# Kernel optimization log

Measured on AMD Instinct MI355X. Metric: run time of the kernel, lower is better.

## Reference

```python
import jax, jax.numpy as jnp
import numpy as np

N = 16384
C_IN = 128
C_OUT = 128
S_DIM = 4
P_DIM = 32
K = 16


def setup_inputs() -> dict:
    key = jax.random.key(0)
    ks = jax.random.split(key, 8)
    lim = lambda fan_in: 1.0 / np.sqrt(fan_in)
    u = lambda k_, shape, b: jax.random.uniform(k_, shape, jnp.float32, -b, b)
    return {
        "x": jax.random.normal(ks[0], (N, C_IN), jnp.float32),
        "Ws": u(ks[1], (S_DIM, C_IN), lim(C_IN)),
        "bs": u(ks[2], (S_DIM,), lim(C_IN)),
        "Wh": u(ks[3], (P_DIM, C_IN), lim(C_IN)),
        "bh": u(ks[4], (P_DIM,), lim(C_IN)),
        "W1": u(ks[5], (C_OUT, C_IN), lim(C_IN)),
        "W2": u(ks[6], (C_OUT, 2 * P_DIM), lim(2 * P_DIM)),
        "b2": u(ks[7], (C_OUT,), lim(2 * P_DIM)),
        "k": K,
    }


def reference(x, Ws, bs, Wh, bh, W1, W2, b2, k):
    # latent space positions and message vectors
    s = x @ Ws.T + bs            # [N, S]
    h = x @ Wh.T + bh            # [N, P]
    # squared-distance matrix via Gram trick (monotone in true distance,
    # so k-NN indices match torch.cdist + topk(largest=False))
    sq = jnp.sum(s * s, axis=-1)                         # [N]
    d2 = sq[:, None] + sq[None, :] - 2.0 * (s @ s.T)     # [N, N]
    _, idx = jax.lax.top_k(-d2, k)                       # [N, k] neighbour ids (incl. self)
    # exact squared latent distance to selected neighbours (as in torch code)
    s_j = s[idx]                                          # [N, k, S]
    w = jnp.exp(-10.0 * jnp.sum((s[:, None, :] - s_j) ** 2, axis=-1))  # [N, k]
    msg = h[idx] * w[..., None]                           # [N, k, P]
    agg = jnp.concatenate([msg.mean(axis=1), msg.max(axis=1)], axis=-1)  # [N, 2P]
    return x @ W1.T + agg @ W2.T + b2                     # [N, C_OUT]
```

## Files before the change

### kernel.cpp

```cpp
#include <hip/hip_runtime.h>
#include <hip/hip_bf16.h>


#define NPTS 16384
#define CIN  128
#define SD   4
#define PD   32
#define KNN  16
#define COUT 128
#define FLTMAX 3.4028234663852886e+38f
#define NBIN 33
#define QPB  8
#define QCAP 512
#define MCAP 192
#define EPAD 1e-3f

typedef float v2f __attribute__((ext_vector_type(2)));
typedef unsigned int uint;
typedef unsigned long long u64;
typedef unsigned short u16;
typedef __attribute__((ext_vector_type(8))) short bf16x8;
typedef __attribute__((ext_vector_type(16))) float f32x16;

#define WS_S4     0
#define WS_H      0x40000
#define WS_AGG_M  0x280000
#define WS_SA     0x280000
#define WS_SB     0x300000
#define WS_WT_M   0x680000
#define WS_MASK   0x700000
#define WS_NEED_M 0x2700000
#define WS_CJ_F   0x400000
#define WS_AGG_F  0xC00000
#define WS_WT_F   0x1000000
#define JS   16
#define TJF  (NPTS/JS)

__device__ __forceinline__ float d2f(const float4 a, const float4 b) {
  v2f d0 = {a.x - b.x, a.y - b.y};
  v2f d1 = {a.z - b.z, a.w - b.w};
  v2f pr = d0*d0 + d1*d1;
  return pr.x + pr.y;
}

__device__ __forceinline__ u16 f2bf(float x) {
  uint u = __float_as_uint(x);
  uint r = (u + 0x7FFFu + ((u >> 16) & 1u)) >> 16;
  return (u16)r;
}
__device__ __forceinline__ float bf2f(u16 h) {
  return __uint_as_float(((uint)h) << 16);
}

__global__ __launch_bounds__(256) void k1_proj(
    const float* __restrict__ x, const float* __restrict__ Ws, const float* __restrict__ bs,
    const float* __restrict__ Wh, const float* __restrict__ bh,
    float4* __restrict__ s4, float* __restrict__ h) {
  __shared__ float  lw[36*128];
  __shared__ float  lx[64*132];
  __shared__ double rs[3*64*5];
  __shared__ float  rh[3*64*33];
  const int t = threadIdx.x;
  const int row0 = blockIdx.x * 64;
  for (int i2 = t; i2 < 36*128; i2 += 256)
    lw[i2] = (i2 < 512) ? Ws[i2] : Wh[i2 - 512];
#pragma unroll
  for (int g = 0; g < 8; ++g) {
    int fi = g*256 + t;
    int r = fi >> 5, c4 = fi & 31;
    *(float4*)&lx[r*132 + c4*4] = *(const float4*)&x[(size_t)(row0 + r)*CIN + c4*4];
  }
  __syncthreads();
  const int kq = t >> 6;
  const int r  = t & 63;
  const int kb = kq * 32;
  double sacc[4] = {0.0, 0.0, 0.0, 0.0};
  float  hacc[32];
#pragma unroll
  for (int p = 0; p < 32; ++p) hacc[p] = 0.f;
#pragma unroll
  for (int k4 = 0; k4 < 8; ++k4) {
    float4 xv = *(const float4*)&lx[r*132 + kb + k4*4];
    int kg = kb + k4*4;
#pragma unroll
    for (int p = 0; p < 4; ++p) {
      float4 wv = *(const float4*)&lw[p*128 + kg];
      sacc[p] = fma((double)xv.x, (double)wv.x, sacc[p]);
      sacc[p] = fma((double)xv.y, (double)wv.y, sacc[p]);
      sacc[p] = fma((double)xv.z, (double)wv.z, sacc[p]);
      sacc[p] = fma((double)xv.w, (double)wv.w, sacc[p]);
    }
#pragma unroll
    for (int p = 0; p < 32; ++p) {
      float4 wv = *(const float4*)&lw[(4+p)*128 + kg];
      hacc[p] = fmaf(xv.x, wv.x, fmaf(xv.y, wv.y, fmaf(xv.z, wv.z, fmaf(xv.w, wv.w, hacc[p]))));
    }
  }
  if (kq > 0) {
    const int bq = kq - 1;
#pragma unroll
    for (int d = 0; d < 4; ++d) rs[(bq*64 + r)*5 + d] = sacc[d];
#pragma unroll
    for (int p = 0; p < 32; ++p) rh[(bq*64 + r)*33 + p] = hacc[p];
  }
  __syncthreads();
  if (kq == 0) {
    const int row = row0 + r;
    float so[4];
#pragma unroll
    for (int d = 0; d < 4; ++d) {
      double sd = sacc[d] + rs[(0*64 + r)*5 + d] + rs[(1*64 + r)*5 + d]
                + rs[(2*64 + r)*5 + d] + (double)bs[d];
      so[d] = (float)sd;
    }
    s4[row] = make_float4(so[0], so[1], so[2], so[3]);
#pragma unroll
    for (int p4 = 0; p4 < 8; ++p4) {
      float o[4];
#pragma unroll
      for (int c = 0; c < 4; ++c) {
        int p = p4*4 + c;
        o[c] = hacc[p] + rh[(0*64 + r)*33 + p] + rh[(1*64 + r)*33 + p]
             + rh[(2*64 + r)*33 + p] + bh[p];
      }
      *(float4*)&h[(size_t)row*PD + p4*4] = make_float4(o[0], o[1], o[2], o[3]);
    }
  }
}

__global__ __launch_bounds__(256) void k2t_thresh(
    const float4* __restrict__ s4, uint4* __restrict__ sA, uint4* __restrict__ sB) {
  __shared__ float4 tile[2064];
  __shared__ uint   lhist[256*NBIN];
  const int t = threadIdx.x;
#pragma unroll
  for (int g = 0; g < 8; ++g) {
    int j = g*256 + t;
    tile[j + (j >> 7)] = s4[j];
  }
#pragma unroll
  for (int b = 0; b < NBIN; ++b) lhist[t*NBIN + b] = 0u;
  const int ql = t >> 4, tq = t & 15;
  const int q  = blockIdx.x*16 + ql;
  const float4 sq = s4[q];
  __syncthreads();
  float tau = d2f(sq, tile[tq*129]);
#pragma unroll
  for (int m = 1; m < 16; m <<= 1) tau = fmaxf(tau, __shfl_xor(tau, m, 16));
  const int ktop = (int)(__float_as_uint(tau) >> 21);
  const int hb = t*NBIN;
#pragma unroll 4
  for (int u = 0; u < 128; ++u) {
    float4 p = tile[tq*129 + u];
    float e = d2f(sq, p);
    int key = (int)(__float_as_uint(e) >> 21);
    int rel = ktop - key;
    rel = rel < 0 ? 0 : (rel > 32 ? 32 : rel);
    atomicAdd(&lhist[hb + rel], 1u);
  }
  __syncthreads();
  uint c0 = 0, c1 = 0;
  const int qb = ql*16;
  for (int u = 0; u < 16; ++u) {
    c0 += lhist[(qb + u)*NBIN + tq*2];
    c1 += (tq*2 + 1 < NBIN) ? lhist[(qb + u)*NBIN + tq*2 + 1] : 0u;
  }
  int S = (int)(c0 + c1);
#pragma unroll
  for (int d = 1; d < 16; d <<= 1) {
    int v = __shfl_down(S, d, 16);
    S += (tq + d < 16) ? v : 0;
  }
  int g = -1;
  if (S >= KNN) g = 2*tq;
  if (S - (int)c0 >= KNN) g = 2*tq + 1;
#pragma unroll
  for (int m = 1; m < 16; m <<= 1) g = max(g, __shfl_xor(g, m, 16));
  if (tq == 0) {
    uint K = (uint)(ktop - g);
    const float tv = __uint_as_float((K << 21) | 0x1FFFFFu);
    float sv[4] = {sq.x, sq.y, sq.z, sq.w};
    const float n2 = sq.x*sq.x + sq.y*sq.y + sq.z*sq.z + sq.w*sq.w;
    u16 hbv[4], lbv[4];
#pragma unroll
    for (int d = 0; d < 4; ++d) {
      u16 hh = f2bf(sv[d]);
      hbv[d] = hh;
      lbv[d] = f2bf(sv[d] - bf2f(hh));
    }
    const float aq = -0.5f*(n2 - tv) + EPAD;
    const float bn = -0.5f*n2;
    u16 aqh = f2bf(aq); u16 aql = f2bf(aq - bf2f(aqh));
    u16 bnh = f2bf(bn); u16 bnl = f2bf(bn - bf2f(bnh));
    const uint oneone = 0x3F803F80u;
    uint a0 = (uint)hbv[0] | ((uint)hbv[1] << 16);
    uint a1 = (uint)hbv[2] | ((uint)hbv[3] << 16);
    uint l0 = (uint)lbv[0] | ((uint)lbv[1] << 16);
    uint l1 = (uint)lbv[2] | ((uint)lbv[3] << 16);
    uint aqw = (uint)aqh | ((uint)aql << 16);
    uint bnw = (uint)bnh | ((uint)bnl << 16);
    uint4 A0; A0.x = a0; A0.y = a1; A0.z = a0; A0.w = a1;
    uint4 A1; A1.x = l0; A1.y = l1; A1.z = oneone; A1.w = aqw;
    uint4 B0; B0.x = a0; B0.y = a1; B0.z = l0; B0.w = l1;
    uint4 B1; B1.x = a0; B1.y = a1; B1.z = bnw; B1.w = oneone;
    sA[(size_t)q*2]     = A0;
    sA[(size_t)q*2 + 1] = A1;
    sB[(size_t)q*2]     = B0;
    sB[(size_t)q*2 + 1] = B1;
  }
}

__device__ __forceinline__ uint packbits16(const f32x16 a, const int shft) {
  uint b[4];
#pragma unroll
  for (int g = 0; g < 4; ++g) {
    uint bg = 0u;
#pragma unroll
    for (int e = 3; e >= 0; --e)
      bg = bg + bg + ((~__float_as_uint(a[4*g + e])) >> 31);
    b[g] = bg;
  }
  return (b[0] | (b[1] << 8) | (b[2] << 16) | (b[3] << 24)) << shft;
}

__global__ __launch_bounds__(256) void k2b_mfma(
    const u16* __restrict__ sA, const u16* __restrict__ sB, uint4* __restrict__ maskw) {
  __shared__ u16 lB[1024*16];
  const int t   = threadIdx.x;
  const int wv  = t >> 6, ln = t & 63;
  const int l31 = ln & 31, hi = ln >> 5;
  const int qbase = (blockIdx.x >> 4) * 256 + wv * 64;
  const int j0    = (blockIdx.x & 15) * 1024;
  for (int r = t; r < 1024; r += 256) {
    const uint4* src = (const uint4*)&sB[(size_t)(j0 + r)*16];
    uint4 v0 = src[0], v1 = src[1];
    *(uint4*)&lB[r*16]     = v0;
    *(uint4*)&lB[r*16 + 8] = v1;
  }
  const bf16x8 qf0 = *(const bf16x8*)&sA[(size_t)(qbase + l31)*16 + hi*8];
  const bf16x8 qf1 = *(const bf16x8*)&sA[(size_t)(qbase + 32 + l31)*16 + hi*8];
  __syncthreads();
  const int sh = hi * 4;
  const f32x16 zc = {0.f,0.f,0.f,0.f,0.f,0.f,0.f,0.f,0.f,0.f,0.f,0.f,0.f,0.f,0.f,0.f};
#pragma unroll 1
  for (int cc = 0; cc < 8; ++cc) {
    uint w0[4], w1[4];
#pragma unroll
    for (int jt = 0; jt < 4; ++jt) {
      const bf16x8 af = *(const bf16x8*)&lB[(cc*128 + jt*32 + l31)*16 + hi*8];
      f32x16 a0 = __builtin_amdgcn_mfma_f32_32x32x16_bf16(af, qf0, zc, 0, 0, 0);
      f32x16 a1 = __builtin_amdgcn_mfma_f32_32x32x16_bf16(af, qf1, zc, 0, 0, 0);
      w0[jt] = packbits16(a0, sh);
      w1[jt] = packbits16(a1, sh);
    }
    uint of[4];
#pragma unroll
    for (int jt = 0; jt < 4; ++jt) {
      uint f0 = w0[jt] | (uint)__shfl_xor((int)w0[jt], 32);
      uint f1 = w1[jt] | (uint)__shfl_xor((int)w1[jt], 32);
      of[jt] = hi ? f1 : f0;
    }
    const int c = (blockIdx.x & 15)*8 + cc;
    uint4 o; o.x = of[0]; o.y = of[1]; o.z = of[2]; o.w = of[3];
    maskw[(size_t)c*NPTS + qbase + ln] = o;
  }
}

__global__ __launch_bounds__(256) void k3_sel2(
    const float4* __restrict__ s4, const float* __restrict__ h,
    const uint4* __restrict__ maskw, float* __restrict__ agg) {
  __shared__ unsigned short jl[QPB*QCAP];
  __shared__ u16  cls[QPB*QCAP];
  __shared__ u64  qbuf[QPB*MCAP];
  __shared__ u64  win[QPB*KNN];
  __shared__ uint hist[QPB*32];
  __shared__ uint cnts[QPB];
  __shared__ uint mc[QPB];
  const int t  = threadIdx.x;
  const int ql = t >> 5, ln = t & 31;
  const int q  = blockIdx.x*QPB + ql;
  if (ln == 0) { cnts[ql] = 0u; mc[ql] = 0u; }
  hist[ql*32 + ln] = 0u;
  if (ln < KNN) win[ql*KNN + ln] = 0ull;
  const float4 sq = s4[q];
  __syncthreads();
  const int qa = t & 7;
  const int cg = t >> 3;
  uint4 m[4];
#pragma unroll
  for (int u = 0; u < 4; ++u)
    m[u] = maskw[(size_t)(cg + u*32)*NPTS + blockIdx.x*QPB + qa];
  int pc = 0;
#pragma unroll
  for (int u = 0; u < 4; ++u)
    pc += __popc(m[u].x) + __popc(m[u].y) + __popc(m[u].z) + __popc(m[u].w);
  int base = (int)atomicAdd(&cnts[qa], (uint)pc);
#pragma unroll
  for (int u = 0; u < 4; ++u) {
    uint wvs[4] = {m[u].x, m[u].y, m[u].z, m[u].w};
#pragma unroll
    for (int w = 0; w < 4; ++w) {
      uint bits = wvs[w];
      const int jb = (cg + u*32)*128 + w*32;
      while (bits) {
        int b = __builtin_ctz(bits); bits &= bits - 1;
        if (base < QCAP) jl[qa*QCAP + base] = (unsigned short)(jb + b);
        ++base;
      }
    }
  }
  __syncthreads();
  const int cnt = min((int)cnts[ql], QCAP);
  uint kmax = 0u;
  {
    int u = ln;
    for (; u + 32 < cnt; u += 64) {
      int ja = jl[ql*QCAP + u];
      int jb = jl[ql*QCAP + u + 32];
      float ea = d2f(sq, s4[ja]);
      float eb = d2f(sq, s4[jb]);
      uint ca = __float_as_uint(ea) >> 21;
      uint cb = __float_as_uint(eb) >> 21;
      cls[ql*QCAP + u]      = (u16)ca;
      cls[ql*QCAP + u + 32] = (u16)cb;
      kmax = max(kmax, max(ca, cb));
    }
    if (u < cnt) {
      int j = jl[ql*QCAP + u];
      float e = d2f(sq, s4[j]);
      uint cv = __float_as_uint(e) >> 21;
      cls[ql*QCAP + u] = (u16)cv;
      kmax = max(kmax, cv);
    }
  }
#pragma unroll
  for (int m2 = 1; m2 < 32; m2 <<= 1) kmax = max(kmax, (uint)__shfl_xor((int)kmax, m2, 32));
  for (int u = ln; u < cnt; u += 32) {
    uint cv = cls[ql*QCAP + u];
    uint rel = min(kmax - cv, 31u);
    atomicAdd(&hist[ql*32 + rel], 1u);
  }
  __syncthreads();
  uint cum = hist[ql*32 + ln];
#pragma unroll
  for (int d = 1; d < 32; d <<= 1) {
    uint v = (uint)__shfl_down((int)cum, d, 32);
    if (ln + d < 32) cum += v;
  }
  const uint need = (uint)(cnt < KNN ? cnt : KNN);
  u64 bal = __ballot(cum >= need);
  uint half = (uint)(bal >> (((t >> 5) & 1) * 32));
  const uint rstar = 31u - (uint)__builtin_clz(half);
  const uint bcls = kmax - rstar;
  __syncthreads();
  for (int u = ln; u < cnt; u += 32) {
    if ((uint)cls[ql*QCAP + u] <= bcls) {
      int j = jl[ql*QCAP + u];
      float e = d2f(sq, s4[j]);
      u64 key = ((u64)__float_as_uint(e) << 14) | (uint)j;
      uint pos = atomicAdd(&mc[ql], 1u);
      if (pos < MCAP) qbuf[ql*MCAP + pos] = key;
    }
  }
  __syncthreads();
  const int mcnt = (int)mc[ql];
  if (mcnt <= MCAP) {
    for (int w = ln; w < mcnt; w += 32) {
      u64 key = qbuf[ql*MCAP + w];
      int rank = 0;
      for (int v = 0; v < mcnt; ++v) rank += (qbuf[ql*MCAP + v] < key) ? 1 : 0;
      if (rank < KNN) win[ql*KNN + rank] = key;
    }
  } else {
    for (int u = ln; u < cnt; u += 32) {
      if ((uint)cls[ql*QCAP + u] <= bcls) {
        int j = jl[ql*QCAP + u];
        float e = d2f(sq, s4[j]);
        u64 key = ((u64)__float_as_uint(e) << 14) | (uint)j;
        int rank = 0;
        for (int v = 0; v < cnt; ++v) {
          int jv = jl[ql*QCAP + v];
          float ev = d2f(sq, s4[jv]);
          u64 kv2 = ((u64)__float_as_uint(ev) << 14) | (uint)jv;
          rank += (kv2 < key) ? 1 : 0;
        }
        if (rank < KNN) win[ql*KNN + rank] = key;
      }
    }
  }
  __syncthreads();
  float sum = 0.f, mx = -FLTMAX;
#pragma unroll
  for (int r4 = 0; r4 < 4; ++r4) {
    u64 k0 = win[ql*KNN + r4*4 + 0];
    u64 k1 = win[ql*KNN + r4*4 + 1];
    u64 k2 = win[ql*KNN + r4*4 + 2];
    u64 k3v = win[ql*KNN + r4*4 + 3];
    int j0 = (int)(k0 & 16383u), j1 = (int)(k1 & 16383u);
    int j2 = (int)(k2 & 16383u), j3 = (int)(k3v & 16383u);
    float h0 = h[(size_t)j0*PD + ln];
    float h1 = h[(size_t)j1*PD + ln];
    float h2 = h[(size_t)j2*PD + ln];
    float h3 = h[(size_t)j3*PD + ln];
    float w0 = __expf(-10.f * __uint_as_float((uint)(k0 >> 14)));
    float w1 = __expf(-10.f * __uint_as_float((uint)(k1 >> 14)));
    float w2 = __expf(-10.f * __uint_as_float((uint)(k2 >> 14)));
    float w3 = __expf(-10.f * __uint_as_float((uint)(k3v >> 14)));
    float m0 = w0*h0, m1 = w1*h1, m2 = w2*h2, m3 = w3*h3;
    sum += m0 + m1 + m2 + m3;
    mx = fmaxf(mx, fmaxf(fmaxf(m0, m1), fmaxf(m2, m3)));
  }
  agg[(size_t)q*64 + ln]      = sum * 0.0625f;
  agg[(size_t)q*64 + 32 + ln] = mx;
}

__global__ __launch_bounds__(256) void k2_knn_fb(
    const float4* __restrict__ s4, unsigned short* __restrict__ cand_j) {
  __shared__ float4 tile[TJF];
  __shared__ int    lbuf[256*33];
  const int t  = threadIdx.x;
  const int ib = blockIdx.x & 31;
  const int jc = blockIdx.x >> 5;
  const int jbase = jc * TJF;
#pragma unroll
  for (int g = 0; g < 4; ++g) tile[g*256 + t] = s4[jbase + g*256 + t];
  const int ia = ib*256 + t;
  const int ic = ia + 8192;
  const float4 sa = s4[ia];
  const float4 sc = s4[ic];
  __syncthreads();
  float va[KNN], vb[KNN]; int ja[KNN], jb[KNN];
#pragma unroll
  for (int q = 0; q < KNN; ++q) { va[q] = FLTMAX; ja[q] = 0; vb[q] = FLTMAX; jb[q] = 0; }
  float cma = FLTMAX, cmb = FLTMAX;
  int cpa = 0, cpb = 0, ca = 0, cb = 0;
  auto insertA = [&](float e, int jj) {
#pragma unroll
    for (int q = 0; q < KNN; ++q) if (q == cpa) { va[q] = e; ja[q] = jj; }
    cma = va[0]; cpa = 0;
#pragma unroll
    for (int q = 1; q < KNN; ++q) { if (va[q] > cma) { cma = va[q]; cpa = q; } }
  };
  auto insertB = [&](float e, int jj) {
#pragma unroll
    for (int q = 0; q < KNN; ++q) if (q == cpb) { vb[q] = e; jb[q] = jj; }
    cmb = vb[0]; cpb = 0;
#pragma unroll
    for (int q = 1; q < KNN; ++q) { if (vb[q] > cmb) { cmb = vb[q]; cpb = q; } }
  };
  auto compactA = [&]() {
    for (int u = 0; u < ca; ++u) {
      int jj = lbuf[t*33 + u];
      float e = d2f(sa, tile[jj]);
      if (e < cma) insertA(e, jj);
    }
    ca = 0;
  };
  auto compactB = [&]() {
    for (int u = 0; u < cb; ++u) {
      int jj = lbuf[t*33 + 16 + u];
      float e = d2f(sc, tile[jj]);
      if (e < cmb) insertB(e, jj);
    }
    cb = 0;
  };
  for (int ob = 0; ob < TJF/8; ++ob) {
#pragma unroll
    for (int u = 0; u < 8; ++u) {
      int jj = ob*8 + u;
      float4 p = tile[jj];
      float ea = d2f(sa, p);
      float eb = d2f(sc, p);
      if (ea < cma) { lbuf[t*33 + ca] = jj; ++ca; }
      if (eb < cmb) { lbuf[t*33 + 16 + cb] = jj; ++cb; }
    }
    if (__any(ca > 8)) compactA();
    if (__any(cb > 8)) compactB();
  }
  compactA(); compactB();
#pragma unroll
  for (int q = 0; q < KNN; ++q) {
    int c = jc*KNN + q;
    cand_j[(size_t)c*NPTS + ia] = (unsigned short)(ja[q] + jbase);
    cand_j[(size_t)c*NPTS + ic] = (unsigned short)(jb[q] + jbase);
  }
}

__global__ __launch_bounds__(256) void k3_merge_fb(
    const float4* __restrict__ s4, const float4* __restrict__ h4,
    const unsigned short* __restrict__ cand_j, float* __restrict__ agg) {
  __shared__ float le[64*67];
  __shared__ int   lj[64*67];
  const int t  = threadIdx.x;
  const int il = t & 63, tq = t >> 6;
  const int i  = blockIdx.x*64 + il;
  const float4 si = s4[i];
  float val[KNN]; int vid[KNN];
#pragma unroll
  for (int q = 0; q < KNN; ++q) { val[q] = FLTMAX; vid[q] = 0; }
  float cmax = FLTMAX; int cpos = 0;
  for (int u = 0; u < 64; ++u) {
    int c = tq*64 + u;
    int j = cand_j[(size_t)c*NPTS + i];
    float e = d2f(si, s4[j]);
    if (e < cmax) {
#pragma unroll
      for (int q = 0; q < KNN; ++q) if (q == cpos) { val[q] = e; vid[q] = j; }
      cmax = val[0]; cpos = 0;
#pragma unroll
      for (int q = 1; q < KNN; ++q) { if (val[q] > cmax) { cmax = val[q]; cpos = q; } }
    }
  }
#pragma unroll
  for (int q = 0; q < KNN; ++q) {
    le[il*67 + tq*16 + q] = val[q];
    lj[il*67 + tq*16 + q] = vid[q];
  }
  __syncthreads();
  if (t < 64) {
    float mv[KNN]; int mj[KNN];
#pragma unroll
    for (int q = 0; q < KNN; ++q) { mv[q] = FLTMAX; mj[q] = 0; }
    float cm2 = FLTMAX; int cp2 = 0;
    for (int u = 0; u < 64; ++u) {
      float e = le[t*67 + u];
      int   j = lj[t*67 + u];
      if (e < cm2) {
#pragma unroll
        for (int q = 0; q < KNN; ++q) if (q == cp2) { mv[q] = e; mj[q] = j; }
        cm2 = mv[0]; cp2 = 0;
#pragma unroll
        for (int q = 1; q < KNN; ++q) { if (mv[q] > cm2) { cm2 = mv[q]; cp2 = q; } }
      }
    }
#pragma unroll
    for (int q = 0; q < KNN; ++q) {
      le[t*67 + q] = __expf(-10.f * mv[q]);
      lj[t*67 + q] = mj[q];
    }
  }
  __syncthreads();
  float ms[8], mm[8];
#pragma unroll
  for (int p = 0; p < 8; ++p) { ms[p] = 0.f; mm[p] = -FLTMAX; }
#pragma unroll 1
  for (int q = 0; q < KNN; ++q) {
    float w = le[il*67 + q];
    int   j = lj[il*67 + q];
    float4 a = h4[(size_t)j*8 + tq*2];
    float4 b = h4[(size_t)j*8 + tq*2 + 1];
    float m0 = a.x*w, m1 = a.y*w, m2 = a.z*w, m3 = a.w*w;
    float m4 = b.x*w, m5 = b.y*w, m6 = b.z*w, m7 = b.w*w;
    ms[0] += m0; mm[0] = fmaxf(mm[0], m0);
    ms[1] += m1; mm[1] = fmaxf(mm[1], m1);
    ms[2] += m2; mm[2] = fmaxf(mm[2], m2);
    ms[3] += m3; mm[3] = fmaxf(mm[3], m3);
    ms[4] += m4; mm[4] = fmaxf(mm[4], m4);
    ms[5] += m5; mm[5] = fmaxf(mm[5], m5);
    ms[6] += m6; mm[6] = fmaxf(mm[6], m6);
    ms[7] += m7; mm[7] = fmaxf(mm[7], m7);
  }
  float4 o0 = make_float4(ms[0]*0.0625f, ms[1]*0.0625f, ms[2]*0.0625f, ms[3]*0.0625f);
  float4 o1 = make_float4(ms[4]*0.0625f, ms[5]*0.0625f, ms[6]*0.0625f, ms[7]*0.0625f);
  *(float4*)&agg[(size_t)i*64 + tq*8]      = o0;
  *(float4*)&agg[(size_t)i*64 + tq*8 + 4]  = o1;
  *(float4*)&agg[(size_t)i*64 + 32 + tq*8]     = make_float4(mm[0], mm[1], mm[2], mm[3]);
  *(float4*)&agg[(size_t)i*64 + 32 + tq*8 + 4] = make_float4(mm[4], mm[5], mm[6], mm[7]);
}

__global__ __launch_bounds__(256) void k4a_wt(
    const float* __restrict__ W1, const float* __restrict__ W2, float* __restrict__ wT) {
  int idx = blockIdx.x*256 + threadIdx.x;
  if (idx >= 192*COUT) return;
  int k = idx >> 7, c = idx & 127;
  float v = (k < 128) ? W1[(size_t)c*128 + k] : W2[(size_t)c*64 + (k - 128)];
  wT[(size_t)k*COUT + c] = v;
}

__global__ __launch_bounds__(256) void k4_out2(
    const float* __restrict__ x, const float* __restrict__ agg,
    const float* __restrict__ wT, const float* __restrict__ b2,
    float* __restrict__ out) {
  __shared__ float xa[32*192];
  const int t = threadIdx.x;
  const int row0 = blockIdx.x * 32;
#pragma unroll
  for (int g = 0; g < 4; ++g) {
    int fi = g*256 + t;
    int r = fi >> 5, c4 = fi & 31;
    *(float4*)&xa[r*192 + c4*4] = *(const float4*)&x[(size_t)(row0+r)*CIN + c4*4];
  }
#pragma unroll
  for (int g = 0; g < 2; ++g) {
    int fi = g*256 + t;
    int r = fi >> 4, c4 = fi & 15;
    *(float4*)&xa[r*192 + 128 + c4*4] = *(const float4*)&agg[(size_t)(row0+r)*64 + c4*4];
  }
  __syncthreads();
  const int c4 = t & 31;
  const int rg = t >> 5;
  float acc[4][4];
#pragma unroll
  for (int r = 0; r < 4; ++r) { acc[r][0]=0.f; acc[r][1]=0.f; acc[r][2]=0.f; acc[r][3]=0.f; }
  for (int k = 0; k < 192; k += 4) {
    float4 w0 = *(const float4*)&wT[(size_t)(k+0)*COUT + c4*4];
    float4 w1 = *(const float4*)&wT[(size_t)(k+1)*COUT + c4*4];
    float4 w2 = *(const float4*)&wT[(size_t)(k+2)*COUT + c4*4];
    float4 w3 = *(const float4*)&wT[(size_t)(k+3)*COUT + c4*4];
#pragma unroll
    for (int r = 0; r < 4; ++r) {
      float4 xv = *(const float4*)&xa[(rg*4 + r)*192 + k];
      acc[r][0] = fmaf(xv.x, w0.x, fmaf(xv.y, w1.x, fmaf(xv.z, w2.x, fmaf(xv.w, w3.x, acc[r][0]))));
      acc[r][1] = fmaf(xv.x, w0.y, fmaf(xv.y, w1.y, fmaf(xv.z, w2.y, fmaf(xv.w, w3.y, acc[r][1]))));
      acc[r][2] = fmaf(xv.x, w0.z, fmaf(xv.y, w1.z, fmaf(xv.z, w2.z, fmaf(xv.w, w3.z, acc[r][2]))));
      acc[r][3] = fmaf(xv.x, w0.w, fmaf(xv.y, w1.w, fmaf(xv.z, w2.w, fmaf(xv.w, w3.w, acc[r][3]))));
    }
  }
  float4 bias = *(const float4*)&b2[c4*4];
#pragma unroll
  for (int r = 0; r < 4; ++r) {
    float4 o = make_float4(acc[r][0]+bias.x, acc[r][1]+bias.y, acc[r][2]+bias.z, acc[r][3]+bias.w);
    *(float4*)&out[(size_t)(row0 + rg*4 + r)*COUT + c4*4] = o;
  }
}

extern "C" void kernel_launch(void* const* d_in, const int* in_sizes, int n_in,
                              void* d_out, int out_size, void* d_ws, size_t ws_size,
                              hipStream_t stream) {
  const float* x  = (const float*)d_in[0];
  const float* Ws = (const float*)d_in[1];
  const float* bs = (const float*)d_in[2];
  const float* Wh = (const float*)d_in[3];
  const float* bh = (const float*)d_in[4];
  const float* W1 = (const float*)d_in[5];
  const float* W2 = (const float*)d_in[6];
  const float* b2 = (const float*)d_in[7];
  float* out = (float*)d_out;

  char* ws = (char*)d_ws;
  float4* s4 = (float4*)(ws + WS_S4);
  float*  h  = (float*) (ws + WS_H);

  k1_proj<<<NPTS/64, 256, 0, stream>>>(x, Ws, bs, Wh, bh, s4, h);

  if (ws_size >= (size_t)WS_NEED_M) {
    float* agg = (float*)(ws + WS_AGG_M);
    float* wT  = (float*)(ws + WS_WT_M);
    uint4* sa  = (uint4*)(ws + WS_SA);
    uint4* sb  = (uint4*)(ws + WS_SB);
    uint4* mw  = (uint4*)(ws + WS_MASK);
    k2t_thresh<<<NPTS/16, 256, 0, stream>>>(s4, sa, sb);
    k2b_mfma<<<1024, 256, 0, stream>>>((const u16*)sa, (const u16*)sb, mw);
    k3_sel2<<<NPTS/QPB, 256, 0, stream>>>(s4, h, (const uint4*)mw, agg);
    k4a_wt<<<(192*COUT + 255)/256, 256, 0, stream>>>(W1, W2, wT);
    k4_out2<<<NPTS/32, 256, 0, stream>>>(x, agg, wT, b2, out);
  } else {
    unsigned short* cj = (unsigned short*)(ws + WS_CJ_F);
    float* agg = (float*)(ws + WS_AGG_F);
    float* wT  = (float*)(ws + WS_WT_F);
    k2_knn_fb<<<512, 256, 0, stream>>>(s4, cj);
    k3_merge_fb<<<NPTS/64, 256, 0, stream>>>(s4, (const float4*)h, cj, agg);
    k4a_wt<<<(192*COUT + 255)/256, 256, 0, stream>>>(W1, W2, wT);
    k4_out2<<<NPTS/32, 256, 0, stream>>>(x, agg, wT, b2, out);
  }
}
```

Baseline: 188.4 us.

## Emit compacted candidate index lists from MFMA kernel instead of dense bitmasks

The MFMA distance kernel now compacts its candidate bits directly into per-query, per-j-chunk index lists (capped at LCAP entries) plus counts, rather than writing a dense 128-word bitmask per query. The selection kernel gathers these lists with a prefix sum over the 16 chunks. When a chunk overflows the cap it rescans that chunk exactly against a stored threshold. This cuts the 32 MB mask write and read and the bit-expansion work in k3. In exchange it adds divergent serial ctz loops and scattered u16 stores in k2b, plus a slow fallback path whenever a chunk overflows.

```diff
diff --git a/kernel.cpp b/kernel.cpp
--- a/kernel.cpp
+++ b/kernel.cpp
@@ -13,6 +13,7 @@
 #define QPB  8
 #define QCAP 512
 #define MCAP 192
+#define LCAP 24
 #define EPAD 1e-3f
 
 typedef float v2f __attribute__((ext_vector_type(2)));
@@ -28,7 +29,9 @@
 #define WS_SA     0x280000
 #define WS_SB     0x300000
 #define WS_WT_M   0x680000
-#define WS_MASK   0x700000
+#define WS_T2     0x6A0000
+#define WS_JLIST  0x700000
+#define WS_JCNT   0x1300000
 #define WS_NEED_M 0x2700000
 #define WS_CJ_F   0x400000
 #define WS_AGG_F  0xC00000
@@ -129,7 +132,8 @@
 }
 
 __global__ __launch_bounds__(256) void k2t_thresh(
-    const float4* __restrict__ s4, uint4* __restrict__ sA, uint4* __restrict__ sB) {
+    const float4* __restrict__ s4, uint4* __restrict__ sA, uint4* __restrict__ sB,
+    float* __restrict__ t2g) {
   __shared__ float4 tile[2064];
   __shared__ uint   lhist[256*NBIN];
   const int t = threadIdx.x;
@@ -179,6 +183,7 @@
   if (tq == 0) {
     uint K = (uint)(ktop - g);
     const float tv = __uint_as_float((K << 21) | 0x1FFFFFu);
+    t2g[q] = tv;
     float sv[4] = {sq.x, sq.y, sq.z, sq.w};
     const float n2 = sq.x*sq.x + sq.y*sq.y + sq.z*sq.z + sq.w*sq.w;
     u16 hbv[4], lbv[4];
@@ -224,13 +229,15 @@
 }
 
 __global__ __launch_bounds__(256) void k2b_mfma(
-    const u16* __restrict__ sA, const u16* __restrict__ sB, uint4* __restrict__ maskw) {
+    const u16* __restrict__ sA, const u16* __restrict__ sB,
+    u16* __restrict__ jlist, u16* __restrict__ jcnt) {
   __shared__ u16 lB[1024*16];
   const int t   = threadIdx.x;
   const int wv  = t >> 6, ln = t & 63;
   const int l31 = ln & 31, hi = ln >> 5;
+  const int jq  = blockIdx.x & 15;
   const int qbase = (blockIdx.x >> 4) * 256 + wv * 64;
-  const int j0    = (blockIdx.x & 15) * 1024;
+  const int j0    = jq * 1024;
   for (int r = t; r < 1024; r += 256) {
     const uint4* src = (const uint4*)&sB[(size_t)(j0 + r)*16];
     uint4 v0 = src[0], v1 = src[1];
@@ -242,6 +249,8 @@
   __syncthreads();
   const int sh = hi * 4;
   const f32x16 zc = {0.f,0.f,0.f,0.f,0.f,0.f,0.f,0.f,0.f,0.f,0.f,0.f,0.f,0.f,0.f,0.f};
+  int cur = 0;
+  const size_t lbase = ((size_t)jq*NPTS + (qbase + ln))*LCAP;
 #pragma unroll 1
   for (int cc = 0; cc < 8; ++cc) {
     uint w0[4], w1[4];
@@ -253,59 +262,99 @@
       w0[jt] = packbits16(a0, sh);
       w1[jt] = packbits16(a1, sh);
     }
-    uint of[4];
 #pragma unroll
     for (int jt = 0; jt < 4; ++jt) {
       uint f0 = w0[jt] | (uint)__shfl_xor((int)w0[jt], 32);
       uint f1 = w1[jt] | (uint)__shfl_xor((int)w1[jt], 32);
-      of[jt] = hi ? f1 : f0;
-    }
-    const int c = (blockIdx.x & 15)*8 + cc;
-    uint4 o; o.x = of[0]; o.y = of[1]; o.z = of[2]; o.w = of[3];
-    maskw[(size_t)c*NPTS + qbase + ln] = o;
-  }
+      uint bits = hi ? f1 : f0;
+      const int jb = j0 + cc*128 + jt*32;
+      while (bits) {
+        int b = __builtin_ctz(bits); bits &= bits - 1;
+        if (cur < LCAP) jlist[lbase + cur] = (u16)(jb + b);
+        ++cur;
+      }
+    }
+  }
+  jcnt[(size_t)jq*NPTS + qbase + ln] = (u16)cur;
 }
 
 __global__ __launch_bounds__(256) void k3_sel2(
     const float4* __restrict__ s4, const float* __restrict__ h,
-    const uint4* __restrict__ maskw, float* __restrict__ agg) {
+    const u16* __restrict__ jlist, const u16* __restrict__ jcnt,
+    const float* __restrict__ t2g, float* __restrict__ agg) {
   __shared__ unsigned short jl[QPB*QCAP];
   __shared__ u16  cls[QPB*QCAP];
   __shared__ u64  qbuf[QPB*MCAP];
   __shared__ u64  win[QPB*KNN];
   __shared__ uint hist[QPB*32];
+  __shared__ uint po[QPB*18];
+  __shared__ uint ovfl[QPB];
   __shared__ uint cnts[QPB];
   __shared__ uint mc[QPB];
   const int t  = threadIdx.x;
   const int ql = t >> 5, ln = t & 31;
   const int q  = blockIdx.x*QPB + ql;
-  if (ln == 0) { cnts[ql] = 0u; mc[ql] = 0u; }
+  if (ln == 0) { mc[ql] = 0u; ovfl[ql] = 0u; }
   hist[ql*32 + ln] = 0u;
   if (ln < KNN) win[ql*KNN + ln] = 0ull;
   const float4 sq = s4[q];
   __syncthreads();
-  const int qa = t & 7;
-  const int cg = t >> 3;
-  uint4 m[4];
-#pragma unroll
-  for (int u = 0; u < 4; ++u)
-    m[u] = maskw[(size_t)(cg + u*32)*NPTS + blockIdx.x*QPB + qa];
-  int pc = 0;
-#pragma unroll
-  for (int u = 0; u < 4; ++u)
-    pc += __popc(m[u].x) + __popc(m[u].y) + __popc(m[u].z) + __popc(m[u].w);
-  int base = (int)atomicAdd(&cnts[qa], (uint)pc);
-#pragma unroll
-  for (int u = 0; u < 4; ++u) {
-    uint wvs[4] = {m[u].x, m[u].y, m[u].z, m[u].w};
-#pragma unroll
-    for (int w = 0; w < 4; ++w) {
-      uint bits = wvs[w];
-      const int jb = (cg + u*32)*128 + w*32;
-      while (bits) {
-        int b = __builtin_ctz(bits); bits &= bits - 1;
-        if (base < QCAP) jl[qa*QCAP + base] = (unsigned short)(jb + b);
-        ++base;
+  uint eff = 0;
+  if (ln < 16) {
+    uint cr = (uint)jcnt[(size_t)ln*NPTS + q];
+    if (cr > (uint)LCAP) { atomicOr(&ovfl[ql], 1u << ln); eff = 0u; }
+    else eff = cr;
+  }
+  uint inc = eff;
+#pragma unroll
+  for (int d = 1; d < 16; d <<= 1) {
+    uint v = (uint)__shfl_up((int)inc, d, 16);
+    if ((ln & 15) >= d) inc += v;
+  }
+  if (ln < 16) po[ql*18 + ln] = inc - eff;
+  if (ln == 15) po[ql*18 + 16] = inc;
+  __syncthreads();
+  const int Tn = (int)po[ql*18 + 16];
+  {
+    int u = ln;
+    for (; u + 32 < Tn; u += 64) {
+      int ua = u, ub = u + 32;
+      int ra = 0, rb = 0;
+#pragma unroll
+      for (int st = 8; st > 0; st >>= 1) {
+        int ca = ra + st, cb2 = rb + st;
+        if (ca <= 15 && (int)po[ql*18 + ca] <= ua) ra = ca;
+        if (cb2 <= 15 && (int)po[ql*18 + cb2] <= ub) rb = cb2;
+      }
+      u16 va = jlist[((size_t)ra*NPTS + q)*LCAP + (ua - (int)po[ql*18 + ra])];
+      u16 vb = jlist[((size_t)rb*NPTS + q)*LCAP + (ub - (int)po[ql*18 + rb])];
+      jl[ql*QCAP + ua] = va;
+      jl[ql*QCAP + ub] = vb;
+    }
+    if (u < Tn) {
+      int r = 0;
+#pragma unroll
+      for (int st = 8; st > 0; st >>= 1) {
+        int c = r + st;
+        if (c <= 15 && (int)po[ql*18 + c] <= u) r = c;
+      }
+      jl[ql*QCAP + u] = jlist[((size_t)r*NPTS + q)*LCAP + (u - (int)po[ql*18 + r])];
+    }
+  }
+  if (ln == 0) cnts[ql] = (uint)Tn;
+  __syncthreads();
+  uint ofm = ovfl[ql];
+  if (ofm) {
+    const float lim = t2g[q] + 2.f*EPAD;
+    while (ofm) {
+      int r = __builtin_ctz(ofm); ofm &= ofm - 1;
+      const int jend = r*1024 + 1024;
+      for (int jj = r*1024 + ln; jj < jend; jj += 32) {
+        float e = d2f(sq, s4[jj]);
+        if (e <= lim) {
+          uint pos = atomicAdd(&cnts[ql], 1u);
+          if (pos < QCAP) jl[ql*QCAP + pos] = (unsigned short)jj;
+        }
       }
     }
   }
@@ -648,10 +697,12 @@
     float* wT  = (float*)(ws + WS_WT_M);
     uint4* sa  = (uint4*)(ws + WS_SA);
     uint4* sb  = (uint4*)(ws + WS_SB);
-    uint4* mw  = (uint4*)(ws + WS_MASK);
-    k2t_thresh<<<NPTS/16, 256, 0, stream>>>(s4, sa, sb);
-    k2b_mfma<<<1024, 256, 0, stream>>>((const u16*)sa, (const u16*)sb, mw);
-    k3_sel2<<<NPTS/QPB, 256, 0, stream>>>(s4, h, (const uint4*)mw, agg);
+    float* t2  = (float*)(ws + WS_T2);
+    u16*   jls = (u16*)  (ws + WS_JLIST);
+    u16*   jcn = (u16*)  (ws + WS_JCNT);
+    k2t_thresh<<<NPTS/16, 256, 0, stream>>>(s4, sa, sb, t2);
+    k2b_mfma<<<1024, 256, 0, stream>>>((const u16*)sa, (const u16*)sb, jls, jcn);
+    k3_sel2<<<NPTS/QPB, 256, 0, stream>>>(s4, h, (const u16*)jls, (const u16*)jcn, t2, agg);
     k4a_wt<<<(192*COUT + 255)/256, 256, 0, stream>>>(W1, W2, wT);
     k4_out2<<<NPTS/32, 256, 0, stream>>>(x, agg, wT, b2, out);
   } else {
```

After: 242.9 us. 28.9% more time.
